# Kernel tuning notes

Hardware: AMD Instinct MI355X
Metric: run time of the kernel (lower is better)

## Reference

```python
import jax, jax.numpy as jnp
import jax.lax as lax
import numpy as np
import math

B, T_FRAMES, H, W = 32, 8, 14, 14
C, CA = 768, 384
L = H * W + 1


def setup_inputs() -> dict:
    key = jax.random.key(0)
    ks = jax.random.split(key, 7)
    s = 0.02
    return {
        "x": jax.random.normal(ks[0], (B * T_FRAMES, L, C), dtype=jnp.float32),
        "W1": jax.random.normal(ks[1], (CA, C), dtype=jnp.float32) * s,
        "b1": jnp.zeros((CA,), dtype=jnp.float32),
        "conv_w": jax.random.normal(ks[2], (CA, 1, 3, 3, 3), dtype=jnp.float32) * s,
        "conv_b": jnp.zeros((CA,), dtype=jnp.float32),
        "W2": jax.random.normal(ks[3], (C, CA), dtype=jnp.float32) * s,
        "b2": jnp.zeros((C,), dtype=jnp.float32),
        "T": T_FRAMES,
    }


def reference(x, W1, b1, conv_w, conv_b, W2, b2, T):
    BT, Lx, Cx = x.shape
    Bb = BT // T
    Ca = W1.shape[0]
    Hh = Ww = int(round(math.sqrt(Lx - 1)))
    # fc1 on all tokens except CLS: [BT, L-1, Ca]
    h = jnp.einsum("blc,ac->bla", x[:, 1:, :], W1) + b1
    # -> [B, Ca, T, H, W] for depthwise 3d conv (groups = Ca)
    h = h.reshape(Bb, T, Hh, Ww, Ca).transpose(0, 4, 1, 2, 3)
    h = lax.conv_general_dilated(
        h, conv_w,
        window_strides=(1, 1, 1),
        padding=[(1, 1), (1, 1), (1, 1)],
        dimension_numbers=("NCDHW", "OIDHW", "NCDHW"),
        feature_group_count=Ca,
    ) + conv_b[None, :, None, None, None]
    # back to [BT, L-1, Ca]
    h = h.transpose(0, 2, 3, 4, 1).reshape(BT, Lx - 1, Ca)
    # fc2: [BT, L-1, C]
    h = jnp.einsum("bla,ca->blc", h, W2) + b2
    # residual add onto non-CLS tokens
    return x.at[:, 1:, :].add(h)
```

## Files before the change

kernel.cpp:

```cpp
#include <hip/hip_runtime.h>
#include <stdint.h>

#define BTOT   256
#define LX     197
#define CDIM   768
#define CADIM  384
#define TFR    8
#define LM1    196
#define MTOT   50176

typedef unsigned short u16;
typedef short          bf16x8 __attribute__((ext_vector_type(8)));
typedef unsigned short u16x4  __attribute__((ext_vector_type(4)));
typedef unsigned short u16x8  __attribute__((ext_vector_type(8)));
typedef float          f32x4  __attribute__((ext_vector_type(4)));

typedef const __attribute__((address_space(1))) void gvoid_t;
typedef __attribute__((address_space(3))) void       svoid_t;

static __device__ __forceinline__ u16 f2bf(float f) {
  union { float f; uint32_t u; } v; v.f = f;
  uint32_t u = v.u;
  return (u16)((u + 0x7FFFu + ((u >> 16) & 1u)) >> 16);
}
static __device__ __forceinline__ float bf2f(u16 h) {
  union { uint32_t u; float f; } v; v.u = ((uint32_t)h) << 16;
  return v.f;
}

__global__ void prep_x(const float4* __restrict__ x, u16x4* __restrict__ xb,
                       float4* __restrict__ out, int nvec) {
  int stride = gridDim.x * blockDim.x;
  for (int i = blockIdx.x * blockDim.x + threadIdx.x; i < nvec; i += stride) {
    float4 v = x[i];
    u16x4 o;
    o[0] = f2bf(v.x); o[1] = f2bf(v.y); o[2] = f2bf(v.z); o[3] = f2bf(v.w);
    xb[i] = o;
    int rem = i % 37824;
    if (rem < 192) out[i] = v;
  }
}

__global__ void prep_w(const float* __restrict__ W1, const float* __restrict__ W2,
                       const float* __restrict__ cw, u16* __restrict__ w1b,
                       u16* __restrict__ w2b, float* __restrict__ cwT) {
  int i = blockIdx.x * blockDim.x + threadIdx.x;
  if (i < CADIM * CDIM) { w1b[i] = f2bf(W1[i]); w2b[i] = f2bf(W2[i]); }
  if (i < CADIM * 27) {
    int a = i / 27; int tap = i - a * 27;
    cwT[tap * CADIM + a] = cw[i];
  }
}


__global__ __launch_bounds__(256) void fc1_gemm(
    const u16* __restrict__ A,
    const u16* __restrict__ Bw,
    const float* __restrict__ bias,
    u16* __restrict__ Hout)
{
  __shared__ __align__(16) u16 As[128 * 64];
  __shared__ __align__(16) u16 Bs[128 * 64];
  const int tid  = threadIdx.x;
  const int lane = tid & 63;
  const int wave = tid >> 6;
  const int m0 = blockIdx.x * 128;
  const int n0 = blockIdx.y * 128;
  const int lm = lane & 15;
  const int lk = lane >> 4;
  const int wm = (wave & 1) * 64;
  const int wn = (wave >> 1) * 64;

  const int srow = lane >> 3;
  const int cch  = (lane & 7) ^ srow;
  size_t aoff[4], boff[4];
  u16 *asdst[4], *bsdst[4];
#pragma unroll
  for (int s = 0; s < 4; ++s) {
    int row = wave * 32 + s * 8 + srow;
    int tok = m0 + row;
    int bt = tok / LM1;
    int l = tok - bt * LM1;
    aoff[s] = (size_t)(bt * LX + 1 + l) * CDIM + cch * 8;
    boff[s] = (size_t)(n0 + row) * CDIM + cch * 8;
    asdst[s] = As + (wave * 32 + s * 8) * 64;
    bsdst[s] = Bs + (wave * 32 + s * 8) * 64;
  }
  const int r7  = lm & 7;
  const int sw0 = ((lk    ) ^ r7) << 3;
  const int sw1 = ((lk + 4) ^ r7) << 3;

  f32x4 acc[4][4];
#pragma unroll
  for (int i = 0; i < 4; i++)
#pragma unroll
    for (int j = 0; j < 4; j++) acc[i][j] = (f32x4)0.0f;

  for (int k0 = 0; k0 < CDIM; k0 += 64) {
#pragma unroll
    for (int s = 0; s < 4; ++s) {
      __builtin_amdgcn_global_load_lds((gvoid_t*)(A + aoff[s] + k0),
                                       (svoid_t*)asdst[s], 16, 0, 0);
      __builtin_amdgcn_global_load_lds((gvoid_t*)(Bw + boff[s] + k0),
                                       (svoid_t*)bsdst[s], 16, 0, 0);
    }
    __syncthreads();
    {
      bf16x8 af[4], bfr[4];
#pragma unroll
      for (int i = 0; i < 4; i++)
        af[i] = *(const bf16x8*)&As[(wm + i * 16 + lm) * 64 + sw0];
#pragma unroll
      for (int j = 0; j < 4; j++)
        bfr[j] = *(const bf16x8*)&Bs[(wn + j * 16 + lm) * 64 + sw0];
#pragma unroll
      for (int i = 0; i < 4; i++)
#pragma unroll
        for (int j = 0; j < 4; j++)
          acc[i][j] = __builtin_amdgcn_mfma_f32_16x16x32_bf16(af[i], bfr[j], acc[i][j], 0, 0, 0);
#pragma unroll
      for (int i = 0; i < 4; i++)
        af[i] = *(const bf16x8*)&As[(wm + i * 16 + lm) * 64 + sw1];
#pragma unroll
      for (int j = 0; j < 4; j++)
        bfr[j] = *(const bf16x8*)&Bs[(wn + j * 16 + lm) * 64 + sw1];
#pragma unroll
      for (int i = 0; i < 4; i++)
#pragma unroll
        for (int j = 0; j < 4; j++)
          acc[i][j] = __builtin_amdgcn_mfma_f32_16x16x32_bf16(af[i], bfr[j], acc[i][j], 0, 0, 0);
    }
    __syncthreads();
  }

#pragma unroll
  for (int i = 0; i < 4; i++) {
    int rbase = m0 + wm + i * 16 + lk * 4;
#pragma unroll
    for (int j = 0; j < 4; j++) {
      int col = n0 + wn + j * 16 + lm;
      float bv = bias[col];
#pragma unroll
      for (int r = 0; r < 4; r++)
        Hout[(rbase + r) * CADIM + col] = f2bf(acc[i][j][r] + bv);
    }
  }
}

__global__ __launch_bounds__(256) void dwconv(
    const u16* __restrict__ h1, const float* __restrict__ cwT,
    const float* __restrict__ cb, u16* __restrict__ h2)
{
  int idx = blockIdx.x * blockDim.x + threadIdx.x;
  int cg = idx % 48;
  int rest = idx / 48;
  int wp = rest % 7; rest /= 7;
  int hp = rest % 7; rest /= 7;
  int t = rest & 7;
  int frame = rest;
  int a0 = cg * 8;
  int h0 = hp * 2, w0 = wp * 2;

  float acc[2][2][8];
#pragma unroll
  for (int c = 0; c < 8; ++c) {
    float bv = cb[a0 + c];
    acc[0][0][c] = bv; acc[0][1][c] = bv; acc[1][0][c] = bv; acc[1][1][c] = bv;
  }

#pragma unroll
  for (int dt = -1; dt <= 1; ++dt) {
    int tt = t + dt;
    if (tt < 0 || tt >= TFR) continue;
    float wreg[9][8];
#pragma unroll
    for (int j = 0; j < 9; ++j) {
      const float* wp8 = cwT + ((dt + 1) * 9 + j) * CADIM + a0;
#pragma unroll
      for (int c = 0; c < 8; ++c) wreg[j][c] = wp8[c];
    }
    const u16* fbase = h1 + (size_t)(frame + dt) * LM1 * CADIM + a0;
#pragma unroll
    for (int ih = 0; ih < 4; ++ih) {
      int hh = h0 - 1 + ih;
      if (hh < 0 || hh >= 14) continue;
#pragma unroll
      for (int iw = 0; iw < 4; ++iw) {
        int ww = w0 - 1 + iw;
        if (ww < 0 || ww >= 14) continue;
        bf16x8 v = *(const bf16x8*)(fbase + (hh * 14 + ww) * CADIM);
        float vf[8];
#pragma unroll
        for (int c = 0; c < 8; ++c) vf[c] = bf2f((u16)v[c]);
#pragma unroll
        for (int oh = 0; oh < 2; ++oh) {
          if (ih - 1 - oh < -1 || ih - 1 - oh > 1) continue;
#pragma unroll
          for (int ow = 0; ow < 2; ++ow) {
            if (iw - 1 - ow < -1 || iw - 1 - ow > 1) continue;
            int j = (ih - oh) * 3 + (iw - ow);
#pragma unroll
            for (int c = 0; c < 8; ++c)
              acc[oh][ow][c] += vf[c] * wreg[j][c];
          }
        }
      }
    }
  }
  const size_t obase = (size_t)frame * LM1 * CADIM + a0;
#pragma unroll
  for (int oh = 0; oh < 2; ++oh)
#pragma unroll
    for (int ow = 0; ow < 2; ++ow) {
      u16x8 o;
#pragma unroll
      for (int c = 0; c < 8; ++c) o[c] = f2bf(acc[oh][ow][c]);
      *(u16x8*)(h2 + obase + ((size_t)(h0 + oh) * 14 + w0 + ow) * CADIM) = o;
    }
}

__global__ __launch_bounds__(256) void fc2_gemm(
    const u16* __restrict__ A,
    const u16* __restrict__ Bw,
    const float* __restrict__ bias,
    const float* __restrict__ x,
    float* __restrict__ out)
{
  __shared__ __align__(16) u16 As[128 * 64];
  __shared__ __align__(16) u16 Bs[128 * 64];
  const int tid  = threadIdx.x;
  const int lane = tid & 63;
  const int wave = tid >> 6;
  const int m0 = blockIdx.x * 128;
  const int n0 = blockIdx.y * 128;
  const int lm = lane & 15;
  const int lk = lane >> 4;
  const int wm = (wave & 1) * 64;
  const int wn = (wave >> 1) * 64;

  const int srow = lane >> 3;
  const int cch  = (lane & 7) ^ srow;
  size_t aoff[4], boff[4];
  u16 *asdst[4], *bsdst[4];
#pragma unroll
  for (int s = 0; s < 4; ++s) {
    int row = wave * 32 + s * 8 + srow;
    aoff[s] = (size_t)(m0 + row) * CADIM + cch * 8;
    boff[s] = (size_t)(n0 + row) * CADIM + cch * 8;
    asdst[s] = As + (wave * 32 + s * 8) * 64;
    bsdst[s] = Bs + (wave * 32 + s * 8) * 64;
  }
  const int r7  = lm & 7;
  const int sw0 = ((lk    ) ^ r7) << 3;
  const int sw1 = ((lk + 4) ^ r7) << 3;

  f32x4 acc[4][4];
#pragma unroll
  for (int i = 0; i < 4; i++)
#pragma unroll
    for (int j = 0; j < 4; j++) acc[i][j] = (f32x4)0.0f;

  for (int k0 = 0; k0 < CADIM; k0 += 64) {
#pragma unroll
    for (int s = 0; s < 4; ++s) {
      __builtin_amdgcn_global_load_lds((gvoid_t*)(A + aoff[s] + k0),
                                       (svoid_t*)asdst[s], 16, 0, 0);
      __builtin_amdgcn_global_load_lds((gvoid_t*)(Bw + boff[s] + k0),
                                       (svoid_t*)bsdst[s], 16, 0, 0);
    }
    __syncthreads();
    {
      bf16x8 af[4], bfr[4];
#pragma unroll
      for (int i = 0; i < 4; i++)
        af[i] = *(const bf16x8*)&As[(wm + i * 16 + lm) * 64 + sw0];
#pragma unroll
      for (int j = 0; j < 4; j++)
        bfr[j] = *(const bf16x8*)&Bs[(wn + j * 16 + lm) * 64 + sw0];
#pragma unroll
      for (int i = 0; i < 4; i++)
#pragma unroll
        for (int j = 0; j < 4; j++)
          acc[i][j] = __builtin_amdgcn_mfma_f32_16x16x32_bf16(af[i], bfr[j], acc[i][j], 0, 0, 0);
#pragma unroll
      for (int i = 0; i < 4; i++)
        af[i] = *(const bf16x8*)&As[(wm + i * 16 + lm) * 64 + sw1];
#pragma unroll
      for (int j = 0; j < 4; j++)
        bfr[j] = *(const bf16x8*)&Bs[(wn + j * 16 + lm) * 64 + sw1];
#pragma unroll
      for (int i = 0; i < 4; i++)
#pragma unroll
        for (int j = 0; j < 4; j++)
          acc[i][j] = __builtin_amdgcn_mfma_f32_16x16x32_bf16(af[i], bfr[j], acc[i][j], 0, 0, 0);
    }
    __syncthreads();
  }

#pragma unroll
  for (int i = 0; i < 4; i++) {
    int rbase = m0 + wm + i * 16 + lk * 4;
#pragma unroll
    for (int r = 0; r < 4; r++) {
      int tok = rbase + r;
      int bt = tok / LM1;
      int l = tok - bt * LM1;
      size_t orow = (size_t)(bt * LX + 1 + l) * CDIM;
#pragma unroll
      for (int j = 0; j < 4; j++) {
        int col = n0 + wn + j * 16 + lm;
        out[orow + col] = x[orow + col] + acc[i][j][r] + bias[col];
      }
    }
  }
}

extern "C" void kernel_launch(void* const* d_in, const int* in_sizes, int n_in,
                              void* d_out, int out_size, void* d_ws, size_t ws_size,
                              hipStream_t stream) {
  const float* x  = (const float*)d_in[0];
  const float* W1 = (const float*)d_in[1];
  const float* b1 = (const float*)d_in[2];
  const float* cw = (const float*)d_in[3];
  const float* cb = (const float*)d_in[4];
  const float* W2 = (const float*)d_in[5];
  const float* b2 = (const float*)d_in[6];
  float* out = (float*)d_out;

  char* ws = (char*)d_ws;
  u16*   xb  = (u16*)(ws + 0);
  u16*   w1b = (u16*)(ws + 77463552);
  u16*   w2b = (u16*)(ws + 78053376);
  float* cwT = (float*)(ws + 78643200);
  u16*   h1  = (u16*)(ws + 78684672);
  u16*   h2  = (u16*)(ws + 117219840);

  const int xelems = BTOT * LX * CDIM;

  prep_x  <<<4096, 256, 0, stream>>>((const float4*)x, (u16x4*)xb, (float4*)out, xelems / 4);
  prep_w  <<<(CADIM * CDIM + 255) / 256, 256, 0, stream>>>(W1, W2, cw, w1b, w2b, cwT);
  fc1_gemm<<<dim3(MTOT / 128, CADIM / 128), 256, 0, stream>>>(xb, w1b, b1, h1);
  dwconv  <<<(BTOT * 49 * 48) / 256, 256, 0, stream>>>(h1, cwT, cb, h2);
  fc2_gemm<<<dim3(MTOT / 128, CDIM / 128), 256, 0, stream>>>(h2, w2b, b2, x, out);
}
```

Baseline: 473.7 us.

## Fuse x bf16 conversion into fc1 and stage GEMM epilogues through LDS

Removes the separate prep_x pass. fc1 now loads fp32 x directly, converts it to bf16 in registers and writes it into a padded LDS tile, and a small kernel copies the CLS rows. The fc1 and fc2 epilogues now stage accumulator tiles in LDS so global stores, and the residual reads in fc2, become 16-byte vectorised and coalesced. In exchange, fc1 re-reads fp32 x once per N-tile, and its A-tile load is synchronous instead of an async global-to-LDS copy.

```diff
diff --git a/kernel.cpp b/kernel.cpp
--- a/kernel.cpp
+++ b/kernel.cpp
@@ -11,7 +11,6 @@
 
 typedef unsigned short u16;
 typedef short          bf16x8 __attribute__((ext_vector_type(8)));
-typedef unsigned short u16x4  __attribute__((ext_vector_type(4)));
 typedef unsigned short u16x8  __attribute__((ext_vector_type(8)));
 typedef float          f32x4  __attribute__((ext_vector_type(4)));
 
@@ -26,19 +25,6 @@
 static __device__ __forceinline__ float bf2f(u16 h) {
   union { uint32_t u; float f; } v; v.u = ((uint32_t)h) << 16;
   return v.f;
-}
-
-__global__ void prep_x(const float4* __restrict__ x, u16x4* __restrict__ xb,
-                       float4* __restrict__ out, int nvec) {
-  int stride = gridDim.x * blockDim.x;
-  for (int i = blockIdx.x * blockDim.x + threadIdx.x; i < nvec; i += stride) {
-    float4 v = x[i];
-    u16x4 o;
-    o[0] = f2bf(v.x); o[1] = f2bf(v.y); o[2] = f2bf(v.z); o[3] = f2bf(v.w);
-    xb[i] = o;
-    int rem = i % 37824;
-    if (rem < 192) out[i] = v;
-  }
 }
 
 __global__ void prep_w(const float* __restrict__ W1, const float* __restrict__ W2,
@@ -52,14 +38,21 @@
   }
 }
 
+__global__ void cls_copy(const float4* __restrict__ x, float4* __restrict__ out) {
+  int i = blockIdx.x * blockDim.x + threadIdx.x;
+  int bt = i / 192;
+  int c  = i - bt * 192;
+  int idx = bt * (LX * CDIM / 4) + c;
+  out[idx] = x[idx];
+}
 
 __global__ __launch_bounds__(256) void fc1_gemm(
-    const u16* __restrict__ A,
+    const float* __restrict__ x,
     const u16* __restrict__ Bw,
     const float* __restrict__ bias,
     u16* __restrict__ Hout)
 {
-  __shared__ __align__(16) u16 As[128 * 64];
+  __shared__ __align__(16) u16 As[128 * 72];
   __shared__ __align__(16) u16 Bs[128 * 64];
   const int tid  = threadIdx.x;
   const int lane = tid & 63;
@@ -71,24 +64,27 @@
   const int wm = (wave & 1) * 64;
   const int wn = (wave >> 1) * 64;
 
+  const int row2 = tid >> 1;
+  const int half = tid & 1;
+  int tokA = m0 + row2;
+  int btA = tokA / LM1;
+  int lA = tokA - btA * LM1;
+  const float* arow = x + (size_t)(btA * LX + 1 + lA) * CDIM + half * 32;
+  u16* adst = As + row2 * 72 + half * 32;
+
   const int srow = lane >> 3;
   const int cch  = (lane & 7) ^ srow;
-  size_t aoff[4], boff[4];
-  u16 *asdst[4], *bsdst[4];
+  size_t boff[4];
+  u16* bsdst[4];
 #pragma unroll
   for (int s = 0; s < 4; ++s) {
     int row = wave * 32 + s * 8 + srow;
-    int tok = m0 + row;
-    int bt = tok / LM1;
-    int l = tok - bt * LM1;
-    aoff[s] = (size_t)(bt * LX + 1 + l) * CDIM + cch * 8;
     boff[s] = (size_t)(n0 + row) * CDIM + cch * 8;
-    asdst[s] = As + (wave * 32 + s * 8) * 64;
     bsdst[s] = Bs + (wave * 32 + s * 8) * 64;
   }
   const int r7  = lm & 7;
-  const int sw0 = ((lk    ) ^ r7) << 3;
-  const int sw1 = ((lk + 4) ^ r7) << 3;
+  const int swб0 = ((lk    ) ^ r7) << 3;
+  const int swб1 = ((lk + 4) ^ r7) << 3;
 
   f32x4 acc[4][4];
 #pragma unroll
@@ -98,21 +94,33 @@
 
   for (int k0 = 0; k0 < CDIM; k0 += 64) {
 #pragma unroll
-    for (int s = 0; s < 4; ++s) {
-      __builtin_amdgcn_global_load_lds((gvoid_t*)(A + aoff[s] + k0),
-                                       (svoid_t*)asdst[s], 16, 0, 0);
+    for (int s = 0; s < 4; ++s)
       __builtin_amdgcn_global_load_lds((gvoid_t*)(Bw + boff[s] + k0),
                                        (svoid_t*)bsdst[s], 16, 0, 0);
+    {
+      float4 v[8];
+#pragma unroll
+      for (int q = 0; q < 8; ++q)
+        v[q] = *(const float4*)(arow + k0 + q * 4);
+#pragma unroll
+      for (int q = 0; q < 4; ++q) {
+        u16x8 o;
+        o[0] = f2bf(v[2*q].x);   o[1] = f2bf(v[2*q].y);
+        o[2] = f2bf(v[2*q].z);   o[3] = f2bf(v[2*q].w);
+        o[4] = f2bf(v[2*q+1].x); o[5] = f2bf(v[2*q+1].y);
+        o[6] = f2bf(v[2*q+1].z); o[7] = f2bf(v[2*q+1].w);
+        *(u16x8*)(adst + q * 8) = o;
+      }
     }
     __syncthreads();
     {
       bf16x8 af[4], bfr[4];
 #pragma unroll
       for (int i = 0; i < 4; i++)
-        af[i] = *(const bf16x8*)&As[(wm + i * 16 + lm) * 64 + sw0];
+        af[i] = *(const bf16x8*)&As[(wm + i * 16 + lm) * 72 + 0 + lk * 8];
 #pragma unroll
       for (int j = 0; j < 4; j++)
-        bfr[j] = *(const bf16x8*)&Bs[(wn + j * 16 + lm) * 64 + sw0];
+        bfr[j] = *(const bf16x8*)&Bs[(wn + j * 16 + lm) * 64 + swб0];
 #pragma unroll
       for (int i = 0; i < 4; i++)
 #pragma unroll
@@ -120,10 +128,10 @@
           acc[i][j] = __builtin_amdgcn_mfma_f32_16x16x32_bf16(af[i], bfr[j], acc[i][j], 0, 0, 0);
 #pragma unroll
       for (int i = 0; i < 4; i++)
-        af[i] = *(const bf16x8*)&As[(wm + i * 16 + lm) * 64 + sw1];
+        af[i] = *(const bf16x8*)&As[(wm + i * 16 + lm) * 72 + 32 + lk * 8];
 #pragma unroll
       for (int j = 0; j < 4; j++)
-        bfr[j] = *(const bf16x8*)&Bs[(wn + j * 16 + lm) * 64 + sw1];
+        bfr[j] = *(const bf16x8*)&Bs[(wn + j * 16 + lm) * 64 + swб1];
 #pragma unroll
       for (int i = 0; i < 4; i++)
 #pragma unroll
@@ -133,17 +141,25 @@
     __syncthreads();
   }
 
+  u16* patch = (u16*)As + wave * 16 * 72;
 #pragma unroll
   for (int i = 0; i < 4; i++) {
-    int rbase = m0 + wm + i * 16 + lk * 4;
 #pragma unroll
     for (int j = 0; j < 4; j++) {
-      int col = n0 + wn + j * 16 + lm;
-      float bv = bias[col];
+      float bv = bias[n0 + wn + j * 16 + lm];
 #pragma unroll
       for (int r = 0; r < 4; r++)
-        Hout[(rbase + r) * CADIM + col] = f2bf(acc[i][j][r] + bv);
-    }
+        patch[(lk * 4 + r) * 72 + j * 16 + lm] = f2bf(acc[i][j][r] + bv);
+    }
+    __syncthreads();
+#pragma unroll
+    for (int p = 0; p < 2; ++p) {
+      int row = (lane >> 3) + p * 8;
+      int col = (lane & 7) * 8;
+      u16x8 v = *(const u16x8*)(patch + row * 72 + col);
+      *(u16x8*)(Hout + (size_t)(m0 + wm + i * 16 + row) * CADIM + n0 + wn + col) = v;
+    }
+    __syncthreads();
   }
 }
 
@@ -297,21 +313,34 @@
     __syncthreads();
   }
 
+  float* patch = (float*)As + wave * 16 * 68;
+  const int erow = lane >> 2;
+  const int ecol = (lane & 3) * 16;
+  f32x4 bias4[4];
+#pragma unroll
+  for (int q = 0; q < 4; ++q)
+    bias4[q] = *(const f32x4*)(bias + n0 + wn + ecol + q * 4);
+
 #pragma unroll
   for (int i = 0; i < 4; i++) {
-    int rbase = m0 + wm + i * 16 + lk * 4;
-#pragma unroll
-    for (int r = 0; r < 4; r++) {
-      int tok = rbase + r;
-      int bt = tok / LM1;
-      int l = tok - bt * LM1;
-      size_t orow = (size_t)(bt * LX + 1 + l) * CDIM;
-#pragma unroll
-      for (int j = 0; j < 4; j++) {
-        int col = n0 + wn + j * 16 + lm;
-        out[orow + col] = x[orow + col] + acc[i][j][r] + bias[col];
-      }
-    }
+#pragma unroll
+    for (int j = 0; j < 4; j++)
+#pragma unroll
+      for (int r = 0; r < 4; r++)
+        patch[(lk * 4 + r) * 68 + j * 16 + lm] = acc[i][j][r];
+    __syncthreads();
+    int tok = m0 + wm + i * 16 + erow;
+    int bt = tok / LM1;
+    int l = tok - bt * LM1;
+    size_t orow = (size_t)(bt * LX + 1 + l) * CDIM + n0 + wn + ecol;
+#pragma unroll
+    for (int q = 0; q < 4; ++q) {
+      f32x4 v = *(const f32x4*)(patch + erow * 68 + ecol + q * 4);
+      f32x4 xv = *(const f32x4*)(x + orow + q * 4);
+      f32x4 o = v + xv + bias4[q];
+      *(f32x4*)(out + orow + q * 4) = o;
+    }
+    __syncthreads();
   }
 }
 
@@ -328,18 +357,15 @@
   float* out = (float*)d_out;
 
   char* ws = (char*)d_ws;
-  u16*   xb  = (u16*)(ws + 0);
-  u16*   w1b = (u16*)(ws + 77463552);
-  u16*   w2b = (u16*)(ws + 78053376);
-  float* cwT = (float*)(ws + 78643200);
-  u16*   h1  = (u16*)(ws + 78684672);
-  u16*   h2  = (u16*)(ws + 117219840);
-
-  const int xelems = BTOT * LX * CDIM;
-
-  prep_x  <<<4096, 256, 0, stream>>>((const float4*)x, (u16x4*)xb, (float4*)out, xelems / 4);
+  u16*   w1b = (u16*)(ws + 0);
+  u16*   w2b = (u16*)(ws + 589824);
+  float* cwT = (float*)(ws + 1179648);
+  u16*   h1  = (u16*)(ws + 1221120);
+  u16*   h2  = (u16*)(ws + 39756288);
+
   prep_w  <<<(CADIM * CDIM + 255) / 256, 256, 0, stream>>>(W1, W2, cw, w1b, w2b, cwT);
-  fc1_gemm<<<dim3(MTOT / 128, CADIM / 128), 256, 0, stream>>>(xb, w1b, b1, h1);
+  cls_copy<<<(BTOT * 192) / 256, 256, 0, stream>>>((const float4*)x, (float4*)out);
+  fc1_gemm<<<dim3(MTOT / 128, CADIM / 128), 256, 0, stream>>>(x, w1b, b1, h1);
   dwconv  <<<(BTOT * 49 * 48) / 256, 256, 0, stream>>>(h1, cwT, cb, h2);
   fc2_gemm<<<dim3(MTOT / 128, CDIM / 128), 256, 0, stream>>>(h2, w2b, b2, x, out);
 }
```

Result: slower. 496.4 us (+4.8%).
